# Performance work log

Hardware: AMD Instinct MI355X
Metric: run time of the kernel (lower is better)

The kernel has to match this reference:

```python
import jax, jax.numpy as jnp
import numpy as np

P, D, Q = 2, 1, 2  # ARIMA(p, d, q) orders from init_kwargs
B_SZ, T_SEQ = 8192, 4096


def setup_inputs() -> dict:
    key = jax.random.key(0)
    k1, k2, k3, k4 = jax.random.split(key, 4)
    y = jax.random.normal(k1, (B_SZ, T_SEQ), dtype=jnp.float32)
    # small coefficients keep the MA recurrence numerically stable
    phi = jax.random.normal(k2, (P,), dtype=jnp.float32) * 0.1
    theta = jax.random.normal(k3, (Q,), dtype=jnp.float32) * 0.1
    mu = jax.random.normal(k4, (1,), dtype=jnp.float32) * 0.1
    return {"y": y, "phi": phi, "theta": theta, "mu": mu}


def reference(y, phi, theta, mu):
    B, Tseq = y.shape
    T = Tseq - D
    yd = y[:, D:] - y[:, :-D]  # d-th difference, (B, T)
    # AR term depends only on y -> precompute for all t in [P, T):
    #   ar[:, t-P] = sum_i phi[i] * y[:, D + t - 1 - i]   (flip + dot)
    ar = jnp.zeros((B, T - P), y.dtype)
    for i in range(P):  # P is tiny and static
        ar = ar + phi[i] * y[:, D + P - 1 - i: D + T - 1 - i]
    target = yd[:, P:] - mu[0] - ar  # (B, T-P): eps_t = target_t - theta . eps_window

    def step(win, tgt):
        eps_t = tgt - win @ theta  # (B,)
        win = jnp.concatenate([eps_t[:, None], win[:, :-1]], axis=1)
        return win, eps_t

    win0 = jnp.zeros((B, Q), y.dtype)  # eps buffer starts at zero
    _, eps_seq = jax.lax.scan(step, win0, target.T)  # (T-P, B)
    eps = eps_seq.T  # (B, T-P)
    # torch code returns eps[:, p:] of the (B, T+q) buffer -> trailing Q zeros
    return jnp.concatenate([eps, jnp.zeros((B, Q), y.dtype)], axis=1)
```

## Files before the change

kernel.cpp:

```cpp
#include <hip/hip_runtime.h>


#define TSEQ  4096
#define TOUT  4095
#define NJ    4093
#define CHUNK 256
#define WARM  64
#define TILE  64
#define PITCH 65

__global__ __launch_bounds__(64) void arima_eps_tiled(
    const float* __restrict__ y,
    const float* __restrict__ phi,
    const float* __restrict__ theta,
    const float* __restrict__ mu,
    float* __restrict__ out, int B)
{
    __shared__ float lds[TILE][PITCH];

    const int lane = threadIdx.x;
    const int g = blockIdx.x >> 4;
    const int c = blockIdx.x & 15;
    const int rowbase = g * 64;
    (void)B;

    const float p0 = phi[0], p1 = phi[1];
    const float q0 = theta[0], q1 = theta[1];
    const float m  = mu[0];

    const float* __restrict__ Y = y + (size_t)rowbase * TSEQ;
    float* __restrict__ O       = out + (size_t)rowbase * TOUT;

    const int j0 = c * CHUNK;
    const int j1 = min(j0 + CHUNK, NJ);
    const int jw = max(j0 - WARM, 0);

    const int lrow = lane >> 4;
    const int lcol = (lane & 15) * 4;

    auto load_tile = [&](int tb) {
        #pragma unroll
        for (int qq = 0; qq < 16; ++qq) {
            const int r = qq * 4 + lrow;
            const float4 v = *reinterpret_cast<const float4*>(
                &Y[(size_t)r * TSEQ + tb + lcol]);
            lds[lcol + 0][r] = v.x;
            lds[lcol + 1][r] = v.y;
            lds[lcol + 2][r] = v.z;
            lds[lcol + 3][r] = v.w;
        }
    };

    float a, b, e1 = 0.f, e2 = 0.f;

    auto step8 = [&](int cb) {
        float yv[8], ev[8];
        #pragma unroll
        for (int k = 0; k < 8; ++k) yv[k] = lds[cb + k][lane];
        #pragma unroll
        for (int k = 0; k < 8; ++k) {
            const float cc  = yv[k];
            const float tgt = cc - b - m - p0 * b - p1 * a;
            const float e   = tgt - q0 * e1 - q1 * e2;
            ev[k] = e;
            e2 = e1; e1 = e; a = b; b = cc;
        }
        #pragma unroll
        for (int k = 0; k < 8; ++k) lds[cb + k][lane] = ev[k];
    };

    auto dump = [&](int jt, int jcur, int tb) {
        const int jd  = max(jt, j0);
        const int je  = min(jcur, j1);
        const int cnt = je - jd;
        if (cnt > 0) {
            const int dcol = jd + 3 - tb;
            float* op = O + jd + lane;
            const bool on = lane < cnt;
            #pragma unroll 8
            for (int r = 0; r < 64; ++r) {
                if (on) op[(size_t)r * TOUT] = lds[dcol + lane][r];
            }
        }
    };

    int tb = jw;
    load_tile(tb);
    __syncthreads();
    {
        float yv[8], ev[5];
        #pragma unroll
        for (int k = 0; k < 8; ++k) yv[k] = lds[k][lane];
        a = yv[1]; b = yv[2];
        #pragma unroll
        for (int k = 3; k < 8; ++k) {
            const float cc  = yv[k];
            const float tgt = cc - b - m - p0 * b - p1 * a;
            const float e   = tgt - q0 * e1 - q1 * e2;
            ev[k - 3] = e;
            e2 = e1; e1 = e; a = b; b = cc;
        }
        #pragma unroll
        for (int k = 3; k < 8; ++k) lds[k][lane] = ev[k - 3];
    }
    #pragma unroll
    for (int cb = 8; cb < 64; cb += 8) step8(cb);
    int j = jw + 61;
    __syncthreads();
    dump(jw, j, tb);

    while (j < j1) {
        __syncthreads();
        tb += TILE;
        load_tile(tb);
        __syncthreads();
        const int jt = j;
        #pragma unroll
        for (int cb = 0; cb < 64; cb += 8) step8(cb);
        j = jt + 64;
        __syncthreads();
        dump(jt, j, tb);
    }

    if (c == 15) {
        O[(size_t)lane * TOUT + NJ]     = 0.f;
        O[(size_t)lane * TOUT + NJ + 1] = 0.f;
    }
}

extern "C" void kernel_launch(void* const* d_in, const int* in_sizes, int n_in,
                              void* d_out, int out_size, void* d_ws, size_t ws_size,
                              hipStream_t stream) {
    const float* y     = (const float*)d_in[0];
    const float* phi   = (const float*)d_in[1];
    const float* theta = (const float*)d_in[2];
    const float* mu    = (const float*)d_in[3];
    float* out         = (float*)d_out;

    int B = in_sizes[0] / TSEQ;
    int rowgroups = B / 64;
    dim3 block(64);
    dim3 grid(rowgroups * 16);
    arima_eps_tiled<<<grid, block, 0, stream>>>(y, phi, theta, mu, out, B);
}
```

Before: 64.28 us.

## Prefetch next tile into registers during dump, halve tile and chunk size

Measured after the change: 117.6 us. +82.9%, slower.

```diff
diff --git a/kernel.cpp b/kernel.cpp
--- a/kernel.cpp
+++ b/kernel.cpp
@@ -1,15 +1,16 @@
 #include <hip/hip_runtime.h>
 
 
-#define TSEQ  4096
-#define TOUT  4095
-#define NJ    4093
-#define CHUNK 256
-#define WARM  64
-#define TILE  64
-#define PITCH 65
+#define TSEQ   4096
+#define TOUT   4095
+#define NJ     4093
+#define CHUNK  128
+#define NCHUNK 32
+#define WARM   61
+#define TILE   32
+#define PITCH  65
 
-__global__ __launch_bounds__(64) void arima_eps_tiled(
+__global__ __launch_bounds__(64, 4) void arima_eps_tiled(
     const float* __restrict__ y,
     const float* __restrict__ phi,
     const float* __restrict__ theta,
@@ -19,8 +20,8 @@
     __shared__ float lds[TILE][PITCH];
 
     const int lane = threadIdx.x;
-    const int g = blockIdx.x >> 4;
-    const int c = blockIdx.x & 15;
+    const int g = blockIdx.x >> 5;
+    const int c = blockIdx.x & (NCHUNK - 1);
     const int rowbase = g * 64;
     (void)B;
 
@@ -35,19 +36,30 @@
     const int j1 = min(j0 + CHUNK, NJ);
     const int jw = max(j0 - WARM, 0);
 
-    const int lrow = lane >> 4;
-    const int lcol = (lane & 15) * 4;
+    const int srow = lane >> 3;
+    const int scol = (lane & 7) << 2;
 
-    auto load_tile = [&](int tb) {
+    float4 stg[8];
+    int sdcol;
+
+    auto stage = [&](int tbase) {
+        int off = tbase + scol;
+        if (off > TSEQ - 4) off = TSEQ - 4;
+        sdcol = off - tbase;
         #pragma unroll
-        for (int qq = 0; qq < 16; ++qq) {
-            const int r = qq * 4 + lrow;
-            const float4 v = *reinterpret_cast<const float4*>(
-                &Y[(size_t)r * TSEQ + tb + lcol]);
-            lds[lcol + 0][r] = v.x;
-            lds[lcol + 1][r] = v.y;
-            lds[lcol + 2][r] = v.z;
-            lds[lcol + 3][r] = v.w;
+        for (int qq = 0; qq < 8; ++qq) {
+            const int r = qq * 8 + srow;
+            stg[qq] = *reinterpret_cast<const float4*>(&Y[(size_t)r * TSEQ + off]);
+        }
+    };
+    auto lds_write = [&]() {
+        #pragma unroll
+        for (int qq = 0; qq < 8; ++qq) {
+            const int r = qq * 8 + srow;
+            lds[sdcol + 0][r] = stg[qq].x;
+            lds[sdcol + 1][r] = stg[qq].y;
+            lds[sdcol + 2][r] = stg[qq].z;
+            lds[sdcol + 3][r] = stg[qq].w;
         }
     };
 
@@ -73,19 +85,21 @@
         const int jd  = max(jt, j0);
         const int je  = min(jcur, j1);
         const int cnt = je - jd;
-        if (cnt > 0) {
-            const int dcol = jd + 3 - tb;
-            float* op = O + jd + lane;
-            const bool on = lane < cnt;
-            #pragma unroll 8
-            for (int r = 0; r < 64; ++r) {
-                if (on) op[(size_t)r * TOUT] = lds[dcol + lane][r];
-            }
+        if (cnt <= 0) return;
+        const int dcol = jd + 3 - tb;
+        const int col  = lane & 31;
+        const int rh   = lane >> 5;
+        const bool on  = col < cnt;
+        #pragma unroll
+        for (int r2 = 0; r2 < 32; ++r2) {
+            const int r = r2 * 2 + rh;
+            if (on) O[(size_t)r * TOUT + jd + col] = lds[dcol + col][r];
         }
     };
 
     int tb = jw;
-    load_tile(tb);
+    stage(tb);
+    lds_write();
     __syncthreads();
     {
         float yv[8], ev[5];
@@ -103,26 +117,25 @@
         #pragma unroll
         for (int k = 3; k < 8; ++k) lds[k][lane] = ev[k - 3];
     }
-    #pragma unroll
-    for (int cb = 8; cb < 64; cb += 8) step8(cb);
-    int j = jw + 61;
-    __syncthreads();
-    dump(jw, j, tb);
+    step8(8); step8(16); step8(24);
+    int jt = jw;
+    int j  = jw + TILE - 3;
 
-    while (j < j1) {
+    for (;;) {
+        const bool more = (j < j1);
+        if (more) stage(tb + TILE);
+        dump(jt, j, tb);
+        if (!more) break;
+        __syncthreads();
+        lds_write();
         __syncthreads();
         tb += TILE;
-        load_tile(tb);
-        __syncthreads();
-        const int jt = j;
-        #pragma unroll
-        for (int cb = 0; cb < 64; cb += 8) step8(cb);
-        j = jt + 64;
-        __syncthreads();
-        dump(jt, j, tb);
+        jt = tb - 3;
+        step8(0); step8(8); step8(16); step8(24);
+        j = jt + TILE;
     }
 
-    if (c == 15) {
+    if (c == NCHUNK - 1) {
         O[(size_t)lane * TOUT + NJ]     = 0.f;
         O[(size_t)lane * TOUT + NJ + 1] = 0.f;
     }
@@ -140,6 +153,6 @@
     int B = in_sizes[0] / TSEQ;
     int rowgroups = B / 64;
     dim3 block(64);
-    dim3 grid(rowgroups * 16);
+    dim3 grid(rowgroups * NCHUNK);
     arima_eps_tiled<<<grid, block, 0, stream>>>(y, phi, theta, mu, out, B);
 }
```
